# Kernel tuning notes

Hardware: AMD Instinct MI355X
Metric: run time of the kernel (lower is better)

Reference implementation:

```python
import jax, jax.numpy as jnp
import numpy as np

B, S, H = 2, 2048, 2048
NH, NKV, HD = 16, 4, 128          # query heads, kv heads, head_dim
THETA = 10000.0


def setup_inputs() -> dict:
    key = jax.random.key(0)
    ks = jax.random.split(key, 9)
    s = 0.02
    return {
        "hidden_states": jax.random.normal(ks[0], (B, S, H), jnp.float32),
        "q_w": jax.random.normal(ks[1], (NH * HD, H), jnp.float32) * s,
        "q_b": jax.random.normal(ks[2], (NH * HD,), jnp.float32) * s,
        "k_w": jax.random.normal(ks[3], (NKV * HD, H), jnp.float32) * s,
        "k_b": jax.random.normal(ks[4], (NKV * HD,), jnp.float32) * s,
        "v_w": jax.random.normal(ks[5], (NKV * HD, H), jnp.float32) * s,
        "v_b": jax.random.normal(ks[6], (NKV * HD,), jnp.float32) * s,
        "o_w": jax.random.normal(ks[7], (H, NH * HD), jnp.float32) * s,
        "o_b": jax.random.normal(ks[8], (H,), jnp.float32) * s,
    }


def _rotate_half(x):
    x1, x2 = jnp.split(x, 2, axis=-1)
    return jnp.concatenate([-x2, x1], axis=-1)


def reference(hidden_states, q_w, q_b, k_w, k_b, v_w, v_b, o_w, o_b):
    b, s, h = hidden_states.shape
    # QKV projections -> (b, heads, s, hd)
    q = (hidden_states @ q_w.T + q_b).reshape(b, s, NH, HD).transpose(0, 2, 1, 3)
    k = (hidden_states @ k_w.T + k_b).reshape(b, s, NKV, HD).transpose(0, 2, 1, 3)
    v = (hidden_states @ v_w.T + v_b).reshape(b, s, NKV, HD).transpose(0, 2, 1, 3)
    # rotary embedding (default position_ids = arange(s))
    pos = jnp.arange(s, dtype=jnp.float32)
    inv_freq = 1.0 / (THETA ** (jnp.arange(0, HD, 2, dtype=jnp.float32) / HD))
    freqs = pos[:, None] * inv_freq[None, :]          # (s, hd/2)
    emb = jnp.concatenate([freqs, freqs], axis=-1)    # (s, hd)
    cos = jnp.cos(emb)[None, None]                    # (1,1,s,hd)
    sin = jnp.sin(emb)[None, None]
    q = q * cos + _rotate_half(q) * sin
    k = k * cos + _rotate_half(k) * sin
    # GQA: repeat kv heads (repeat_interleave along head dim)
    n_rep = NH // NKV
    k = jnp.repeat(k, n_rep, axis=1)
    v = jnp.repeat(v, n_rep, axis=1)
    # attention (mathematically what the chunked online-softmax intends)
    scores = jnp.einsum('bhqd,bhkd->bhqk', q, k) / np.sqrt(HD).astype(np.float32)
    m = jnp.max(scores, axis=-1, keepdims=True)
    e = jnp.exp(scores - m)
    attn = jnp.einsum('bhqk,bhkd->bhqd', e, v) / (jnp.sum(e, axis=-1, keepdims=True) + 1e-10)
    attn = attn.transpose(0, 2, 1, 3).reshape(b, s, NH * HD)
    return attn @ o_w.T + o_b
```

## Files before the change

### kernel.cpp

```cpp
#include <hip/hip_runtime.h>
#include <hip/hip_bf16.h>
#include <math.h>

typedef __attribute__((ext_vector_type(8))) short bf16x8;
typedef __attribute__((ext_vector_type(4))) float f32x4;
typedef __attribute__((ext_vector_type(16))) float f32x16;
typedef __attribute__((ext_vector_type(4))) unsigned int u32x4;

#if __has_builtin(__builtin_amdgcn_exp2f)
#define EXP2(x) __builtin_amdgcn_exp2f(x)
#else
#define EXP2(x) __expf((x) * 0.6931471805599453f)
#endif

__device__ __forceinline__ ushort f2bf(float f) {
  unsigned u = __float_as_uint(f);
  u = u + 0x7FFFu + ((u >> 16) & 1u);
  return (ushort)(u >> 16);
}
__device__ __forceinline__ float bf2f(ushort h) {
  return __uint_as_float(((unsigned)h) << 16);
}
__device__ __forceinline__ unsigned cvtpk(float a, float b) {
  unsigned r;
  asm("v_cvt_pk_bf16_f32 %0, %1, %2" : "=v"(r) : "v"(a), "v"(b));
  return r;
}
__device__ __forceinline__ void gload_lds16(const ushort* g, ushort* l) {
  __builtin_amdgcn_global_load_lds((const __attribute__((address_space(1))) void*)g,
                                   (__attribute__((address_space(3))) void*)l, 16, 0, 0);
}

__global__ __launch_bounds__(256) void prep_kernel(
    const float* __restrict__ hs, const float* __restrict__ qw,
    const float* __restrict__ kw, const float* __restrict__ vw,
    const float* __restrict__ ow, const float* __restrict__ qb,
    const float* __restrict__ kb, const float* __restrict__ vb,
    ushort* __restrict__ hs_b, ushort* __restrict__ qkvw_b,
    ushort* __restrict__ ow_b, float* __restrict__ qkvb,
    float2* __restrict__ rope_tab)
{
  const int idx = blockIdx.x * 256 + threadIdx.x;
  const int stride = gridDim.x * 256;
  const float4* hs4 = (const float4*)hs;
  const float4* qw4 = (const float4*)qw;
  const float4* kw4 = (const float4*)kw;
  const float4* vw4 = (const float4*)vw;
  const float4* ow4 = (const float4*)ow;
  ushort4* hsb4 = (ushort4*)hs_b;
  ushort4* qkvwb4 = (ushort4*)qkvw_b;
  ushort4* owb4 = (ushort4*)ow_b;

  for (int i = idx; i < 2097152; i += stride) {
    float4 v = hs4[i];
    ushort4 o; o.x=f2bf(v.x); o.y=f2bf(v.y); o.z=f2bf(v.z); o.w=f2bf(v.w);
    hsb4[i] = o;
  }
  for (int i = idx; i < 1048576; i += stride) {
    float4 v = qw4[i];
    ushort4 o; o.x=f2bf(v.x); o.y=f2bf(v.y); o.z=f2bf(v.z); o.w=f2bf(v.w);
    qkvwb4[i] = o;
  }
  for (int i = idx; i < 262144; i += stride) {
    float4 v = kw4[i];
    ushort4 o; o.x=f2bf(v.x); o.y=f2bf(v.y); o.z=f2bf(v.z); o.w=f2bf(v.w);
    qkvwb4[1048576 + i] = o;
  }
  for (int i = idx; i < 262144; i += stride) {
    float4 v = vw4[i];
    ushort4 o; o.x=f2bf(v.x); o.y=f2bf(v.y); o.z=f2bf(v.z); o.w=f2bf(v.w);
    qkvwb4[1310720 + i] = o;
  }
  for (int i = idx; i < 1048576; i += stride) {
    float4 v = ow4[i];
    ushort4 o; o.x=f2bf(v.x); o.y=f2bf(v.y); o.z=f2bf(v.z); o.w=f2bf(v.w);
    owb4[i] = o;
  }
  for (int i = idx; i < 3072; i += stride)
    qkvb[i] = (i < 2048) ? qb[i] : (i < 2560 ? kb[i - 2048] : vb[i - 2560]);
  for (int i = idx; i < 131072; i += stride) {
    int pos = i >> 6, d = i & 63;
    float inv = __expf((float)d * -0.14391156831212787f);
    float ang = (float)pos * inv;
    rope_tab[i] = make_float2(cosf(ang), sinf(ang));
  }
}

template<int MODE>
__global__ __launch_bounds__(512, 2) void gemm256(
    const ushort* __restrict__ A, const ushort* __restrict__ Bw,
    const float* __restrict__ bias, void* __restrict__ out,
    ushort* __restrict__ vt, const float2* __restrict__ tab)
{
  __shared__ ushort smem[32768];
  const int tid = threadIdx.x;
  const int lane = tid & 63, wid = tid >> 6;
  const int wr = wid >> 2, wc = wid & 3;
  const int qd = lane >> 4, ln = lane & 15;
  const long row0 = (long)blockIdx.x * 256, col0 = (long)blockIdx.y * 256;
  const long K = 2048;

  int pcolF[4];
#pragma unroll
  for (int ni = 0; ni < 4; ni++)
    pcolF[ni] = MODE ? (8 * (wc >> 1) + 2 * (wc & 1) + (ni & 1) + (ni >> 1) * 4)
                     : (wc * 4 + ni);

  f32x4 acc[8][4];
#pragma unroll
  for (int i = 0; i < 8; i++)
#pragma unroll
    for (int j = 0; j < 4; j++) acc[i][j] = (f32x4){0.f, 0.f, 0.f, 0.f};

  const ushort* gA = A + (row0 + (tid >> 2)) * K + (tid & 3) * 8;
  const ushort* gB = Bw + (col0 + (tid >> 2)) * K + (tid & 3) * 8;
  const long R128 = 128 * K;
  const int tid8 = tid * 8;

  gload_lds16(gA,        smem + tid8);
  gload_lds16(gA + R128, smem + 4096 + tid8);
  gload_lds16(gB,        smem + 8192 + tid8);
  gload_lds16(gB + R128, smem + 12288 + tid8);

  for (int kt = 0; kt < 2048; kt += 32) {
    const int st = (kt >> 5) & 1;
    const ushort* As = smem + st * 16384;
    const ushort* Bs = As + 8192;
    ushort* Dst = smem + (st ^ 1) * 16384;
    const bool more = (kt + 32) < 2048;

    if (more) {
      gload_lds16(gA + kt + 32,        Dst + tid8);
      gload_lds16(gA + kt + 32 + R128, Dst + 4096 + tid8);
      asm volatile("s_waitcnt vmcnt(2)" ::: "memory");
    } else {
      asm volatile("s_waitcnt vmcnt(0)" ::: "memory");
    }
    __builtin_amdgcn_s_barrier();
    asm volatile("" ::: "memory");
    bf16x8 bf[4], af[4];
#pragma unroll
    for (int ni = 0; ni < 4; ni++)
      bf[ni] = *(const bf16x8*)&Bs[(pcolF[ni] * 16 + ln) * 32 + qd * 8];
#pragma unroll
    for (int mi = 0; mi < 4; mi++)
      af[mi] = *(const bf16x8*)&As[(wr * 128 + mi * 16 + ln) * 32 + qd * 8];
    __builtin_amdgcn_s_setprio(1);
#pragma unroll
    for (int mi = 0; mi < 4; mi++)
#pragma unroll
      for (int ni = 0; ni < 4; ni++)
        acc[mi][ni] = __builtin_amdgcn_mfma_f32_16x16x32_bf16(af[mi], bf[ni], acc[mi][ni], 0, 0, 0);
    __builtin_amdgcn_s_setprio(0);

    bf16x8 ag[4];
#pragma unroll
    for (int mi = 0; mi < 4; mi++)
      ag[mi] = *(const bf16x8*)&As[(wr * 128 + 64 + mi * 16 + ln) * 32 + qd * 8];
    if (more) {
      gload_lds16(gB + kt + 32,        Dst + 8192 + tid8);
      gload_lds16(gB + kt + 32 + R128, Dst + 12288 + tid8);
    }
    __builtin_amdgcn_s_setprio(1);
#pragma unroll
    for (int mi = 0; mi < 4; mi++)
#pragma unroll
      for (int ni = 0; ni < 4; ni++)
        acc[mi + 4][ni] = __builtin_amdgcn_mfma_f32_16x16x32_bf16(ag[mi], bf[ni], acc[mi + 4][ni], 0, 0, 0);
    __builtin_amdgcn_s_setprio(0);
    asm volatile("" ::: "memory");
    __builtin_amdgcn_s_barrier();
    asm volatile("" ::: "memory");
  }

  float bv[4];
#pragma unroll
  for (int ni = 0; ni < 4; ni++) bv[ni] = bias[col0 + pcolF[ni] * 16 + ln];

  if (MODE == 0) {
    float* C = (float*)out;
#pragma unroll
    for (int j = 0; j < 8; j++)
#pragma unroll
      for (int ni = 0; ni < 4; ni++)
#pragma unroll
        for (int r = 0; r < 4; r++) {
          long row = row0 + wr * 128 + j * 16 + qd * 4 + r;
          long col = col0 + pcolF[ni] * 16 + ln;
          C[row * 2048 + col] = acc[j][ni][r] + bv[ni];
        }
  } else if (col0 >= 2560) {
#pragma unroll
    for (int j = 0; j < 8; j++)
#pragma unroll
      for (int ni = 0; ni < 4; ni++)
#pragma unroll
        for (int r = 0; r < 4; r++) {
          long row = row0 + wr * 128 + j * 16 + qd * 4 + r;
          long col = col0 + pcolF[ni] * 16 + ln - 2560;
          vt[col * 4096 + row] = f2bf(acc[j][ni][r] + bv[ni]);
        }
  } else {
    ushort* qkbuf = (ushort*)out;
    const float sc = (col0 < 2048) ? 0.12751744399764505f : 1.0f;
    const long hbase = col0 + (wc >> 1) * 128;
#pragma unroll
    for (int j = 0; j < 8; j++)
#pragma unroll
      for (int ni = 0; ni < 2; ni++) {
        const int d = (2 * (wc & 1) + ni) * 16 + ln;
#pragma unroll
        for (int r = 0; r < 4; r++) {
          long row = row0 + wr * 128 + j * 16 + qd * 4 + r;
          int pos = (int)(row & 2047);
          float2 cs = tab[pos * 64 + d];
          float c = cs.x * sc, s = cs.y * sc;
          float v0 = acc[j][ni][r]     + bv[ni];
          float v1 = acc[j][ni + 2][r] + bv[ni + 2];
          ushort* p = qkbuf + row * 2560 + hbase + d;
          p[0]  = f2bf(v0 * c - v1 * s);
          p[64] = f2bf(v1 * c + v0 * s);
        }
      }
  }
}

__global__ __launch_bounds__(256, 2) void flash_kernel(
    const ushort* __restrict__ qk, const ushort* __restrict__ vt,
    ushort* __restrict__ ctx)
{
  __shared__ ushort smem[32768];
  const int t = threadIdx.x, lane = t & 63, wv = t >> 6;
  const int h2 = lane >> 5, m = lane & 31;
  const int q0 = blockIdx.x * 128;
  const int b = blockIdx.y >> 4, h = blockIdx.y & 15;
  const long rb = (long)b * 2048;
  const ushort* Qg  = qk + (rb + q0) * 2560 + h * 128;
  const ushort* Kg  = qk + rb * 2560 + 2048 + (h >> 2) * 128;
  const ushort* Vtg = vt + ((long)(h >> 2) * 128) * 4096 + rb;

  bf16x8 qf[8];
  {
    const ushort* qrow = Qg + (long)(wv * 32 + m) * 2560 + h2 * 8;
#pragma unroll
    for (int s2 = 0; s2 < 8; s2++)
      qf[s2] = *(const bf16x8*)(qrow + s2 * 16);
  }

  f32x16 oacc[4];
#pragma unroll
  for (int d = 0; d < 4; d++)
#pragma unroll
    for (int r = 0; r < 16; r++) oacc[d][r] = 0.f;
  float l_run = 0.f;

  const ushort* gK[4];
  const ushort* gV[4];
#pragma unroll
  for (int s = 0; s < 4; s++) {
    int krow = wv * 16 + s * 4 + (lane >> 4);
    int kcd  = (lane & 15) ^ (krow & 15);
    gK[s] = Kg + (long)krow * 2560 + kcd * 8;
    int vrow = wv * 32 + s * 8 + (lane >> 3);
    int vcd  = (lane & 7) ^ ((lane >> 3) & 7);
    gV[s] = Vtg + (long)vrow * 4096 + vcd * 8;
  }
  const int ldsK = wv * 16 * 128;
  const int ldsV = 8192 + wv * 32 * 64;

#pragma unroll
  for (int s = 0; s < 4; s++) gload_lds16(gK[s], smem + ldsK + s * 512);
#pragma unroll
  for (int s = 0; s < 4; s++) gload_lds16(gV[s], smem + ldsV + s * 512);
#pragma unroll
  for (int s = 0; s < 4; s++) { gK[s] += 64l * 2560; gV[s] += 64; }

  const int mk = (m & 15);
  const int mv = (m & 7);

  for (int kt = 0; kt < 2048; kt += 64) {
    const int cb = (kt >> 6) & 1;
    __syncthreads();
    if (kt < 1984) {
      ushort* nb = smem + (cb ^ 1) * 16384;
#pragma unroll
      for (int s = 0; s < 4; s++) gload_lds16(gK[s], nb + ldsK + s * 512);
#pragma unroll
      for (int s = 0; s < 4; s++) gload_lds16(gV[s], nb + ldsV + s * 512);
#pragma unroll
      for (int s = 0; s < 4; s++) { gK[s] += 64l * 2560; gV[s] += 64; }
    }
    const ushort* KsB  = smem + cb * 16384;
    const ushort* VtsB = KsB + 8192;

    float s_sum = 0.f;
#pragma unroll
    for (int kb = 0; kb < 2; kb++) {
      f32x16 sacc;
#pragma unroll
      for (int r = 0; r < 16; r++) sacc[r] = 0.f;
      __builtin_amdgcn_s_setprio(1);
#pragma unroll
      for (int s2 = 0; s2 < 8; s2++) {
        bf16x8 kf = *(const bf16x8*)&KsB[(32 * kb + m) * 128 + ((s2 * 2 + h2) ^ mk) * 8];
        sacc = __builtin_amdgcn_mfma_f32_32x32x16_bf16(kf, qf[s2], sacc, 0, 0, 0);
      }
      __builtin_amdgcn_s_setprio(0);
#pragma unroll
      for (int sh = 0; sh < 2; sh++) {
        float e0 = EXP2(sacc[8 * sh + 0]);
        float e1 = EXP2(sacc[8 * sh + 1]);
        float e2 = EXP2(sacc[8 * sh + 2]);
        float e3 = EXP2(sacc[8 * sh + 3]);
        float e4 = EXP2(sacc[8 * sh + 4]);
        float e5 = EXP2(sacc[8 * sh + 5]);
        float e6 = EXP2(sacc[8 * sh + 6]);
        float e7 = EXP2(sacc[8 * sh + 7]);
        s_sum += ((e0 + e1) + (e2 + e3)) + ((e4 + e5) + (e6 + e7));
        unsigned u0 = cvtpk(e0, e1);
        unsigned u1 = cvtpk(e2, e3);
        unsigned u2 = cvtpk(e4, e5);
        unsigned u3 = cvtpk(e6, e7);
        auto r0 = __builtin_amdgcn_permlane32_swap(u0, u2, false, false);
        auto r1 = __builtin_amdgcn_permlane32_swap(u1, u3, false, false);
        u32x4 pu;
        pu.x = r0[0];
        pu.y = r1[0];
        pu.z = r0[1];
        pu.w = r1[1];
        bf16x8 pfv = __builtin_bit_cast(bf16x8, pu);
        const int s = 2 * kb + sh;
        __builtin_amdgcn_s_setprio(1);
#pragma unroll
        for (int db = 0; db < 4; db++) {
          bf16x8 vf = *(const bf16x8*)&VtsB[(db * 32 + m) * 64 + ((s * 2 + h2) ^ mv) * 8];
          oacc[db] = __builtin_amdgcn_mfma_f32_32x32x16_bf16(vf, pfv, oacc[db], 0, 0, 0);
        }
        __builtin_amdgcn_s_setprio(0);
      }
    }
    l_run += s_sum + __int_as_float(__shfl_xor(__float_as_int(s_sum), 32, 64));
  }

  const float linv = 1.f / (l_run + 1e-10f);
  __syncthreads();
  ushort* Obuf = smem;
#pragma unroll
  for (int db = 0; db < 4; db++)
#pragma unroll
    for (int r = 0; r < 16; r++) {
      int d = db * 32 + (r & 3) + 8 * (r >> 2) + 4 * h2;
      Obuf[(wv * 32 + m) * 136 + d] = f2bf(oacc[db][r] * linv);
    }
  __syncthreads();
  {
    int qr = t >> 1;
    ushort* dst = ctx + (rb + q0 + qr) * 2048 + h * 128;
#pragma unroll
    for (int c = 0; c < 8; c++) {
      int off = ((t & 1) * 8 + c) * 8;
      *(uint4*)(dst + off) = *(const uint4*)&Obuf[qr * 136 + off];
    }
  }
}

extern "C" void kernel_launch(void* const* d_in, const int* in_sizes, int n_in,
                              void* d_out, int out_size, void* d_ws, size_t ws_size,
                              hipStream_t stream)
{
  const float* hs = (const float*)d_in[0];
  const float* qw = (const float*)d_in[1];
  const float* qb = (const float*)d_in[2];
  const float* kw = (const float*)d_in[3];
  const float* kb = (const float*)d_in[4];
  const float* vw = (const float*)d_in[5];
  const float* vb = (const float*)d_in[6];
  const float* ow = (const float*)d_in[7];
  const float* ob = (const float*)d_in[8];

  char* ws = (char*)d_ws;
  ushort* hs_b   = (ushort*)(ws);
  ushort* qkvw_b = (ushort*)(ws + 16777216);
  ushort* ow_b   = (ushort*)(ws + 29360128);
  float*  qkvb   = (float*) (ws + 37748736);
  ushort* qkbuf  = (ushort*)(ws + 37761024);
  ushort* vtbuf  = (ushort*)(ws + 58732544);
  ushort* ctx    = (ushort*)(ws + 62926848);
  float2* rope_tab = (float2*)(ws + 62926848);

  prep_kernel<<<1024, 256, 0, stream>>>(hs, qw, kw, vw, ow, qb, kb, vb,
                                        hs_b, qkvw_b, ow_b, qkvb, rope_tab);
  gemm256<1><<<dim3(16, 12), 512, 0, stream>>>(hs_b, qkvw_b, qkvb, (void*)qkbuf,
                                               vtbuf, rope_tab);
  flash_kernel<<<dim3(16, 32), 256, 0, stream>>>(qkbuf, vtbuf, ctx);
  gemm256<0><<<dim3(16, 8), 512, 0, stream>>>(ctx, ow_b, ob, d_out,
                                              nullptr, nullptr);
}
```

Measured before the change: 329.7 us.

## Shrink projection GEMM tiles to 128x128 with 2-wave blocks for more CTAs

Replaces the 256x256 tile, 8-wave GEMM with a 128x128 tile, 2-wave kernel where each wave computes a 64x128 slab. The grid grows from 192/128 blocks to 768/512 so the 256 CUs get better coverage, and the RoPE epilogue is remapped so each block's 128 columns hold one full head. The cost is less data reuse per tile, meaning more global and LDS traffic per FLOP, and fewer waves per block to hide latency.

Result: faster. 306.8 us (median of 2 runs) (-7.0%).

```diff
diff --git a/kernel.cpp b/kernel.cpp
--- a/kernel.cpp
+++ b/kernel.cpp
@@ -87,137 +87,130 @@
 }
 
 template<int MODE>
-__global__ __launch_bounds__(512, 2) void gemm256(
+__global__ __launch_bounds__(128, 2) void gemm128(
     const ushort* __restrict__ A, const ushort* __restrict__ Bw,
     const float* __restrict__ bias, void* __restrict__ out,
     ushort* __restrict__ vt, const float2* __restrict__ tab)
 {
-  __shared__ ushort smem[32768];
+  __shared__ ushort smem[2][8192];
   const int tid = threadIdx.x;
-  const int lane = tid & 63, wid = tid >> 6;
-  const int wr = wid >> 2, wc = wid & 3;
+  const int lane = tid & 63, wv = tid >> 6;
   const int qd = lane >> 4, ln = lane & 15;
-  const long row0 = (long)blockIdx.x * 256, col0 = (long)blockIdx.y * 256;
-  const long K = 2048;
-
-  int pcolF[4];
-#pragma unroll
-  for (int ni = 0; ni < 4; ni++)
-    pcolF[ni] = MODE ? (8 * (wc >> 1) + 2 * (wc & 1) + (ni & 1) + (ni >> 1) * 4)
-                     : (wc * 4 + ni);
-
-  f32x4 acc[8][4];
-#pragma unroll
-  for (int i = 0; i < 8; i++)
-#pragma unroll
-    for (int j = 0; j < 4; j++) acc[i][j] = (f32x4){0.f, 0.f, 0.f, 0.f};
-
-  const ushort* gA = A + (row0 + (tid >> 2)) * K + (tid & 3) * 8;
-  const ushort* gB = Bw + (col0 + (tid >> 2)) * K + (tid & 3) * 8;
-  const long R128 = 128 * K;
+  const long row0 = (long)blockIdx.x * 128, col0 = (long)blockIdx.y * 128;
+
+  f32x4 acc[4][8];
+#pragma unroll
+  for (int i = 0; i < 4; i++)
+#pragma unroll
+    for (int j = 0; j < 8; j++) acc[i][j] = (f32x4){0.f, 0.f, 0.f, 0.f};
+
+  const ushort* gA = A + (row0 + (tid >> 2)) * 2048l + (tid & 3) * 8;
+  const ushort* gB = Bw + (col0 + (tid >> 2)) * 2048l + (tid & 3) * 8;
+  const long R32 = 32l * 2048;
   const int tid8 = tid * 8;
 
-  gload_lds16(gA,        smem + tid8);
-  gload_lds16(gA + R128, smem + 4096 + tid8);
-  gload_lds16(gB,        smem + 8192 + tid8);
-  gload_lds16(gB + R128, smem + 12288 + tid8);
+#pragma unroll
+  for (int i = 0; i < 4; i++) gload_lds16(gA + i * R32, &smem[0][i * 1024 + tid8]);
+#pragma unroll
+  for (int i = 0; i < 4; i++) gload_lds16(gB + i * R32, &smem[0][4096 + i * 1024 + tid8]);
 
   for (int kt = 0; kt < 2048; kt += 32) {
     const int st = (kt >> 5) & 1;
-    const ushort* As = smem + st * 16384;
-    const ushort* Bs = As + 8192;
-    ushort* Dst = smem + (st ^ 1) * 16384;
+    const ushort* As = smem[st];
+    const ushort* Bs = As + 4096;
+    ushort* Dst = smem[st ^ 1];
     const bool more = (kt + 32) < 2048;
 
     if (more) {
-      gload_lds16(gA + kt + 32,        Dst + tid8);
-      gload_lds16(gA + kt + 32 + R128, Dst + 4096 + tid8);
-      asm volatile("s_waitcnt vmcnt(2)" ::: "memory");
+#pragma unroll
+      for (int i = 0; i < 4; i++)
+        gload_lds16(gA + kt + 32 + i * R32, Dst + i * 1024 + tid8);
+      asm volatile("s_waitcnt vmcnt(4)" ::: "memory");
     } else {
       asm volatile("s_waitcnt vmcnt(0)" ::: "memory");
     }
     __builtin_amdgcn_s_barrier();
     asm volatile("" ::: "memory");
-    bf16x8 bf[4], af[4];
-#pragma unroll
-    for (int ni = 0; ni < 4; ni++)
-      bf[ni] = *(const bf16x8*)&Bs[(pcolF[ni] * 16 + ln) * 32 + qd * 8];
-#pragma unroll
-    for (int mi = 0; mi < 4; mi++)
-      af[mi] = *(const bf16x8*)&As[(wr * 128 + mi * 16 + ln) * 32 + qd * 8];
+    bf16x8 bf[8], af[2];
+#pragma unroll
+    for (int ni = 0; ni < 8; ni++)
+      bf[ni] = *(const bf16x8*)&Bs[(ni * 16 + ln) * 32 + qd * 8];
+#pragma unroll
+    for (int mi = 0; mi < 2; mi++)
+      af[mi] = *(const bf16x8*)&As[(wv * 64 + mi * 16 + ln) * 32 + qd * 8];
     __builtin_amdgcn_s_setprio(1);
 #pragma unroll
-    for (int mi = 0; mi < 4; mi++)
-#pragma unroll
-      for (int ni = 0; ni < 4; ni++)
+    for (int mi = 0; mi < 2; mi++)
+#pragma unroll
+      for (int ni = 0; ni < 8; ni++)
         acc[mi][ni] = __builtin_amdgcn_mfma_f32_16x16x32_bf16(af[mi], bf[ni], acc[mi][ni], 0, 0, 0);
     __builtin_amdgcn_s_setprio(0);
 
-    bf16x8 ag[4];
-#pragma unroll
-    for (int mi = 0; mi < 4; mi++)
-      ag[mi] = *(const bf16x8*)&As[(wr * 128 + 64 + mi * 16 + ln) * 32 + qd * 8];
+    bf16x8 ag[2];
+#pragma unroll
+    for (int mi = 0; mi < 2; mi++)
+      ag[mi] = *(const bf16x8*)&As[(wv * 64 + 32 + mi * 16 + ln) * 32 + qd * 8];
     if (more) {
-      gload_lds16(gB + kt + 32,        Dst + 8192 + tid8);
-      gload_lds16(gB + kt + 32 + R128, Dst + 12288 + tid8);
+#pragma unroll
+      for (int i = 0; i < 4; i++)
+        gload_lds16(gB + kt + 32 + i * R32, Dst + 4096 + i * 1024 + tid8);
     }
     __builtin_amdgcn_s_setprio(1);
 #pragma unroll
-    for (int mi = 0; mi < 4; mi++)
-#pragma unroll
-      for (int ni = 0; ni < 4; ni++)
-        acc[mi + 4][ni] = __builtin_amdgcn_mfma_f32_16x16x32_bf16(ag[mi], bf[ni], acc[mi + 4][ni], 0, 0, 0);
+    for (int mi = 0; mi < 2; mi++)
+#pragma unroll
+      for (int ni = 0; ni < 8; ni++)
+        acc[mi + 2][ni] = __builtin_amdgcn_mfma_f32_16x16x32_bf16(ag[mi], bf[ni], acc[mi + 2][ni], 0, 0, 0);
     __builtin_amdgcn_s_setprio(0);
     asm volatile("" ::: "memory");
     __builtin_amdgcn_s_barrier();
     asm volatile("" ::: "memory");
   }
 
-  float bv[4];
-#pragma unroll
-  for (int ni = 0; ni < 4; ni++) bv[ni] = bias[col0 + pcolF[ni] * 16 + ln];
+  float bv[8];
+#pragma unroll
+  for (int ni = 0; ni < 8; ni++) bv[ni] = bias[col0 + ni * 16 + ln];
 
   if (MODE == 0) {
     float* C = (float*)out;
 #pragma unroll
-    for (int j = 0; j < 8; j++)
-#pragma unroll
-      for (int ni = 0; ni < 4; ni++)
+    for (int mi = 0; mi < 4; mi++)
+#pragma unroll
+      for (int ni = 0; ni < 8; ni++)
 #pragma unroll
         for (int r = 0; r < 4; r++) {
-          long row = row0 + wr * 128 + j * 16 + qd * 4 + r;
-          long col = col0 + pcolF[ni] * 16 + ln;
-          C[row * 2048 + col] = acc[j][ni][r] + bv[ni];
+          long row = row0 + wv * 64 + mi * 16 + qd * 4 + r;
+          long col = col0 + ni * 16 + ln;
+          C[row * 2048 + col] = acc[mi][ni][r] + bv[ni];
         }
   } else if (col0 >= 2560) {
 #pragma unroll
-    for (int j = 0; j < 8; j++)
-#pragma unroll
-      for (int ni = 0; ni < 4; ni++)
+    for (int mi = 0; mi < 4; mi++)
+#pragma unroll
+      for (int ni = 0; ni < 8; ni++)
 #pragma unroll
         for (int r = 0; r < 4; r++) {
-          long row = row0 + wr * 128 + j * 16 + qd * 4 + r;
-          long col = col0 + pcolF[ni] * 16 + ln - 2560;
-          vt[col * 4096 + row] = f2bf(acc[j][ni][r] + bv[ni]);
+          long row = row0 + wv * 64 + mi * 16 + qd * 4 + r;
+          long col = col0 + ni * 16 + ln - 2560;
+          vt[col * 4096 + row] = f2bf(acc[mi][ni][r] + bv[ni]);
         }
   } else {
     ushort* qkbuf = (ushort*)out;
     const float sc = (col0 < 2048) ? 0.12751744399764505f : 1.0f;
-    const long hbase = col0 + (wc >> 1) * 128;
-#pragma unroll
-    for (int j = 0; j < 8; j++)
-#pragma unroll
-      for (int ni = 0; ni < 2; ni++) {
-        const int d = (2 * (wc & 1) + ni) * 16 + ln;
+#pragma unroll
+    for (int mi = 0; mi < 4; mi++)
+#pragma unroll
+      for (int ni = 0; ni < 4; ni++) {
+        const int d = ni * 16 + ln;
 #pragma unroll
         for (int r = 0; r < 4; r++) {
-          long row = row0 + wr * 128 + j * 16 + qd * 4 + r;
+          long row = row0 + wv * 64 + mi * 16 + qd * 4 + r;
           int pos = (int)(row & 2047);
           float2 cs = tab[pos * 64 + d];
           float c = cs.x * sc, s = cs.y * sc;
-          float v0 = acc[j][ni][r]     + bv[ni];
-          float v1 = acc[j][ni + 2][r] + bv[ni + 2];
-          ushort* p = qkbuf + row * 2560 + hbase + d;
+          float v0 = acc[mi][ni][r]     + bv[ni];
+          float v1 = acc[mi][ni + 4][r] + bv[ni + 4];
+          ushort* p = qkbuf + row * 2560 + col0 + d;
           p[0]  = f2bf(v0 * c - v1 * s);
           p[64] = f2bf(v1 * c + v0 * s);
         }
@@ -390,9 +383,9 @@
 
   prep_kernel<<<1024, 256, 0, stream>>>(hs, qw, kw, vw, ow, qb, kb, vb,
                                         hs_b, qkvw_b, ow_b, qkvb, rope_tab);
-  gemm256<1><<<dim3(16, 12), 512, 0, stream>>>(hs_b, qkvw_b, qkvb, (void*)qkbuf,
+  gemm128<1><<<dim3(32, 24), 128, 0, stream>>>(hs_b, qkvw_b, qkvb, (void*)qkbuf,
                                                vtbuf, rope_tab);
   flash_kernel<<<dim3(16, 32), 256, 0, stream>>>(qkbuf, vtbuf, ctx);
-  gemm256<0><<<dim3(16, 8), 512, 0, stream>>>(ctx, ow_b, ob, d_out,
-                                              nullptr, nullptr);
-}
+  gemm128<0><<<dim3(32, 16), 128, 0, stream>>>(ctx, ow_b, ob, d_out,
+                                               nullptr, nullptr);
+}
```
